# Kernel optimization log

Hardware: AMD Instinct MI355X
Metric: run time of the kernel (lower is better)

Reference implementation:

```python
import jax, jax.numpy as jnp
import numpy as np

D_MODEL = 1024
D_FF = 286
NUM_REL = 2
EPS = 1e-6


def setup_inputs() -> dict:
    key = jax.random.key(0)
    ks = jax.random.split(key, 8)
    N, E = 20000, 320000
    hidden_states = jax.random.normal(ks[0], (N, D_MODEL), dtype=jnp.float32)
    edge_index = jax.random.randint(ks[1], (2, E), 0, N, dtype=jnp.int64)
    edge_type = jax.random.randint(ks[2], (E,), 0, NUM_REL, dtype=jnp.int64)
    # learned parameters
    ln_weight = jnp.ones((D_MODEL,), dtype=jnp.float32)
    W_rel = jax.random.normal(ks[3], (NUM_REL, D_MODEL, D_FF), dtype=jnp.float32) * (1.0 / np.sqrt(D_MODEL))
    W_root = jax.random.normal(ks[4], (D_MODEL, D_FF), dtype=jnp.float32) * (1.0 / np.sqrt(D_MODEL))
    conv_bias = jnp.zeros((D_FF,), dtype=jnp.float32)
    wo_weight = jax.random.normal(ks[5], (D_FF, D_MODEL), dtype=jnp.float32) * (1.0 / np.sqrt(D_FF))
    return {"hidden_states": hidden_states, "edge_index": edge_index, "edge_type": edge_type,
            "ln_weight": ln_weight, "W_rel": W_rel, "W_root": W_root,
            "conv_bias": conv_bias, "wo_weight": wo_weight}


def t5_layer_norm(x, weight):
    # T5-style: RMS only, no mean subtraction, no bias; variance in fp32
    var = jnp.mean(jnp.square(x.astype(jnp.float32)), axis=-1, keepdims=True)
    return weight * (x * jax.lax.rsqrt(var + EPS))


def rgcn_conv(x, edge_index, edge_type, W_rel, W_root, bias):
    # PyG RGCNConv with aggr='mean' per relation, root weight, bias.
    N = x.shape[0]
    src, dst = edge_index[0], edge_index[1]
    h_src = x[src]  # [E, d_model] gather
    out = x @ W_root + bias  # root term, [N, d_ff]
    for r in range(NUM_REL):
        w = (edge_type == r).astype(x.dtype)  # [E]
        msg = (h_src @ W_rel[r]) * w[:, None]  # [E, d_ff]
        sums = jax.ops.segment_sum(msg, dst, num_segments=N)  # [N, d_ff]
        cnt = jax.ops.segment_sum(w, dst, num_segments=N)  # [N]
        out = out + sums / jnp.maximum(cnt, 1.0)[:, None]
    return out


def reference(hidden_states, edge_index, edge_type, ln_weight, W_rel, W_root, conv_bias, wo_weight):
    norm_x = t5_layer_norm(hidden_states, ln_weight)
    y = jax.nn.elu(rgcn_conv(norm_x, edge_index, edge_type, W_rel, W_root, conv_bias))
    # dropout layers are identity in eval mode
    y = y @ wo_weight  # [N, d_model], Linear(d_ff, d_model, bias=False)
    return hidden_states + y
```

## Files before the change

kernel.cpp:

```cpp
#include <hip/hip_runtime.h>
#include <hip/hip_bf16.h>


typedef __bf16  bf16x8  __attribute__((ext_vector_type(8)));
typedef float   floatx4 __attribute__((ext_vector_type(4)));

#define NNODE   20000
#define DMODEL  1024
#define DFF     286
#define DFFP    288
#define NDW     144
#define NPAIR   72

typedef __attribute__((address_space(1))) const void* gptr_t;
typedef __attribute__((address_space(3))) void*       lptr_t;

struct alignas(8) bf4 { __bf16 x, y, z, w; };

__device__ __forceinline__ float bflo(unsigned u) {
    union { unsigned u; float f; } c; c.u = u << 16; return c.f;
}
__device__ __forceinline__ float bfhi(unsigned u) {
    union { unsigned u; float f; } c; c.u = u & 0xffff0000u; return c.f;
}
__device__ __forceinline__ unsigned packbf(float a, float b) {
    union { __bf16 h[2]; unsigned u; } c;
    c.h[0] = (__bf16)a; c.h[1] = (__bf16)b; return c.u;
}
__device__ __forceinline__ float elu1(float v) {
    return v > 0.0f ? v : (expf(v) - 1.0f);
}

__global__ __launch_bounds__(256) void k_transpose_cast(
    const float* __restrict__ src, __bf16* __restrict__ dst,
    int K, int N, int Kout, int Nout)
{
    __shared__ float t[32][33];
    int tx = threadIdx.x & 31, ty = threadIdx.x >> 5;
    int k0 = blockIdx.x * 32, n0 = blockIdx.y * 32;
    #pragma unroll
    for (int r = 0; r < 4; ++r) {
        int k = k0 + ty + r * 8, n = n0 + tx;
        t[ty + r * 8][tx] = (k < K && n < N) ? src[(size_t)k * N + n] : 0.0f;
    }
    __syncthreads();
    #pragma unroll
    for (int r = 0; r < 4; ++r) {
        int n = n0 + ty + r * 8, k = k0 + tx;
        if (n < Nout && k < Kout) dst[(size_t)n * Kout + k] = (__bf16)t[tx][ty + r * 8];
    }
}

__global__ __launch_bounds__(256) void k_rmsnorm(
    const float* __restrict__ x, const float* __restrict__ w,
    __bf16* __restrict__ out)
{
    int row = blockIdx.x;
    int t = threadIdx.x;
    float4 v = reinterpret_cast<const float4*>(x + (size_t)row * DMODEL)[t];
    float ss = v.x * v.x + v.y * v.y + v.z * v.z + v.w * v.w;
    #pragma unroll
    for (int off = 32; off; off >>= 1) ss += __shfl_down(ss, off, 64);
    __shared__ float red[4];
    int lane = t & 63, wv = t >> 6;
    if (lane == 0) red[wv] = ss;
    __syncthreads();
    float tot = red[0] + red[1] + red[2] + red[3];
    float scale = rsqrtf(tot * (1.0f / (float)DMODEL) + 1e-6f);
    float4 wv4 = reinterpret_cast<const float4*>(w)[t];
    bf4 o;
    o.x = (__bf16)(v.x * scale * wv4.x);
    o.y = (__bf16)(v.y * scale * wv4.y);
    o.z = (__bf16)(v.z * scale * wv4.z);
    o.w = (__bf16)(v.w * scale * wv4.w);
    reinterpret_cast<bf4*>(out + (size_t)row * DMODEL)[t] = o;
}

__global__ __launch_bounds__(256, 2) void k_gemm1(
    const __bf16* __restrict__ A, const __bf16* __restrict__ Broot,
    const __bf16* __restrict__ Brel, __bf16* __restrict__ P)
{
    const int bid = blockIdx.x;
    const int mt = bid / 3, mz = bid - mt * 3;
    const __bf16* B = (mz == 0) ? Broot : (Brel + (size_t)(mz - 1) * DFFP * DMODEL);
    __bf16* out = P + (size_t)mz * NNODE * DFFP;

    const int m0 = mt * 128;
    const int tid = threadIdx.x;
    const int lane = tid & 63, wave = tid >> 6;
    const int wm = wave >> 1, wn = wave & 1;
    const int quad = lane >> 4, l16 = lane & 15;

    __shared__ __align__(16) __bf16 As[128 * 32];
    __shared__ __align__(16) __bf16 Bs[288 * 32];

    floatx4 zero = {0.f, 0.f, 0.f, 0.f};
    floatx4 acc[4][9];
    #pragma unroll
    for (int i = 0; i < 4; ++i)
        #pragma unroll
        for (int j = 0; j < 9; ++j) acc[i][j] = zero;

    const int crow = lane >> 2;
    const int ccol = (lane & 3) * 8;

    for (int k0 = 0; k0 < DMODEL; k0 += 32) {
        #pragma unroll
        for (int ii = 0; ii < 7; ++ii) {
            int c = wave + ii * 4;
            if (c < 8) {
                int row = c * 16 + crow;
                int grow = m0 + row; if (grow > NNODE - 1) grow = NNODE - 1;
                __builtin_amdgcn_global_load_lds(
                    (gptr_t)(A + (size_t)grow * DMODEL + k0 + ccol),
                    (lptr_t)(As + c * 512), 16, 0, 0);
            } else if (c < 26) {
                int nrow = (c - 8) * 16 + crow;
                __builtin_amdgcn_global_load_lds(
                    (gptr_t)(B + (size_t)nrow * DMODEL + k0 + ccol),
                    (lptr_t)(Bs + (c - 8) * 512), 16, 0, 0);
            }
        }
        __syncthreads();
        bf16x8 af[4], bq[9];
        #pragma unroll
        for (int i = 0; i < 4; ++i)
            af[i] = *reinterpret_cast<const bf16x8*>(As + (wm * 64 + i * 16 + l16) * 32 + quad * 8);
        #pragma unroll
        for (int j = 0; j < 9; ++j)
            bq[j] = *reinterpret_cast<const bf16x8*>(Bs + (wn * 144 + j * 16 + l16) * 32 + quad * 8);
        #pragma unroll
        for (int i = 0; i < 4; ++i)
            #pragma unroll
            for (int j = 0; j < 9; ++j)
                acc[i][j] = __builtin_amdgcn_mfma_f32_16x16x32_bf16(af[i], bq[j], acc[i][j], 0, 0, 0);
        __syncthreads();
    }
    #pragma unroll
    for (int i = 0; i < 4; ++i) {
        int rbase = m0 + wm * 64 + i * 16 + quad * 4;
        #pragma unroll
        for (int j = 0; j < 9; ++j) {
            int col = wn * 144 + j * 16 + l16;
            #pragma unroll
            for (int rr = 0; rr < 4; ++rr) {
                int row = rbase + rr;
                if (row < NNODE) out[(size_t)row * DFFP + col] = (__bf16)acc[i][j][rr];
            }
        }
    }
}

__global__ __launch_bounds__(256) void k_hist(
    const int* __restrict__ ei, int* __restrict__ bcnt, int E)
{
    int t = blockIdx.x * 256 + threadIdx.x;
    if (t < E) atomicAdd(&bcnt[ei[E + t]], 1);
}

__global__ __launch_bounds__(1024) void k_scan(
    const int* __restrict__ bcnt, int* __restrict__ boff, int* __restrict__ bcur)
{
    const int CH = 20;
    __shared__ int s[1024];
    int t = threadIdx.x;
    int base = t * CH;
    int loc[CH];
    int sum = 0;
    #pragma unroll
    for (int i = 0; i < CH; ++i) {
        int idx = base + i;
        int v = (idx < NNODE) ? bcnt[idx] : 0;
        loc[i] = sum; sum += v;
    }
    s[t] = sum;
    __syncthreads();
    for (int off = 1; off < 1024; off <<= 1) {
        int v = (t >= off) ? s[t - off] : 0;
        __syncthreads();
        s[t] += v;
        __syncthreads();
    }
    int prev = (t == 0) ? 0 : s[t - 1];
    #pragma unroll
    for (int i = 0; i < CH; ++i) {
        int idx = base + i;
        if (idx < NNODE) { int o = prev + loc[i]; boff[idx] = o; bcur[idx] = o; }
    }
    if (t == 1023) boff[NNODE] = s[1023];
}

__global__ __launch_bounds__(256) void k_scatter_idx(
    const int* __restrict__ ei, const int* __restrict__ et,
    int* __restrict__ bcur, int* __restrict__ sorted, int E)
{
    int t = blockIdx.x * 256 + threadIdx.x;
    if (t >= E) return;
    int src = ei[t], dst = ei[E + t], r = et[t];
    int pos = atomicAdd(&bcur[dst], 1);
    sorted[pos] = src | (r << 20);
}

__global__ __launch_bounds__(256) void k_reduce(
    const int* __restrict__ boff, const int* __restrict__ sorted,
    const __bf16* __restrict__ proj, const float* __restrict__ bias,
    __bf16* __restrict__ y2)
{
    int b = blockIdx.x * 4 + (threadIdx.x >> 6);
    int lane = threadIdx.x & 63;
    int start = boff[b], end = boff[b + 1];
    bool t8 = lane < 8;

    const uint2* base1 = reinterpret_cast<const uint2*>(proj + (size_t)NNODE * DFFP);
    const uint2* base2 = reinterpret_cast<const uint2*>(proj + (size_t)2 * NNODE * DFFP);

    float a0[4] = {0.f, 0.f, 0.f, 0.f}, a0t[4] = {0.f, 0.f, 0.f, 0.f};
    float a1[4] = {0.f, 0.f, 0.f, 0.f}, a1t[4] = {0.f, 0.f, 0.f, 0.f};
    int c0 = 0, c1 = 0;
    uint2 zz; zz.x = 0u; zz.y = 0u;

    int e = start;
    for (; e + 2 <= end; e += 2) {
        int p0 = sorted[e], p1 = sorted[e + 1];
        int r0i = p0 >> 20, r1i = p1 >> 20;
        const uint2* r0 = (r0i ? base2 : base1) + (size_t)(p0 & 0xFFFFF) * NPAIR;
        const uint2* r1 = (r1i ? base2 : base1) + (size_t)(p1 & 0xFFFFF) * NPAIR;
        uint2 x0 = r0[lane];
        uint2 x1 = r1[lane];
        uint2 y0 = t8 ? r0[64 + lane] : zz;
        uint2 y1 = t8 ? r1[64 + lane] : zz;
        if (r0i) {
            a1[0] += bflo(x0.x); a1[1] += bfhi(x0.x); a1[2] += bflo(x0.y); a1[3] += bfhi(x0.y);
            a1t[0] += bflo(y0.x); a1t[1] += bfhi(y0.x); a1t[2] += bflo(y0.y); a1t[3] += bfhi(y0.y);
            ++c1;
        } else {
            a0[0] += bflo(x0.x); a0[1] += bfhi(x0.x); a0[2] += bflo(x0.y); a0[3] += bfhi(x0.y);
            a0t[0] += bflo(y0.x); a0t[1] += bfhi(y0.x); a0t[2] += bflo(y0.y); a0t[3] += bfhi(y0.y);
            ++c0;
        }
        if (r1i) {
            a1[0] += bflo(x1.x); a1[1] += bfhi(x1.x); a1[2] += bflo(x1.y); a1[3] += bfhi(x1.y);
            a1t[0] += bflo(y1.x); a1t[1] += bfhi(y1.x); a1t[2] += bflo(y1.y); a1t[3] += bfhi(y1.y);
            ++c1;
        } else {
            a0[0] += bflo(x1.x); a0[1] += bfhi(x1.x); a0[2] += bflo(x1.y); a0[3] += bfhi(x1.y);
            a0t[0] += bflo(y1.x); a0t[1] += bfhi(y1.x); a0t[2] += bflo(y1.y); a0t[3] += bfhi(y1.y);
            ++c0;
        }
    }
    if (e < end) {
        int p0 = sorted[e];
        int r0i = p0 >> 20;
        const uint2* r0 = (r0i ? base2 : base1) + (size_t)(p0 & 0xFFFFF) * NPAIR;
        uint2 x0 = r0[lane];
        uint2 y0 = t8 ? r0[64 + lane] : zz;
        if (r0i) {
            a1[0] += bflo(x0.x); a1[1] += bfhi(x0.x); a1[2] += bflo(x0.y); a1[3] += bfhi(x0.y);
            a1t[0] += bflo(y0.x); a1t[1] += bfhi(y0.x); a1t[2] += bflo(y0.y); a1t[3] += bfhi(y0.y);
            ++c1;
        } else {
            a0[0] += bflo(x0.x); a0[1] += bfhi(x0.x); a0[2] += bflo(x0.y); a0[3] += bfhi(x0.y);
            a0t[0] += bflo(y0.x); a0t[1] += bfhi(y0.x); a0t[2] += bflo(y0.y); a0t[3] += bfhi(y0.y);
            ++c0;
        }
    }

    float inv0 = 1.0f / fmaxf((float)c0, 1.0f);
    float inv1 = 1.0f / fmaxf((float)c1, 1.0f);

    const uint2* rootrow = reinterpret_cast<const uint2*>(proj) + (size_t)b * NPAIR;
    uint2* outrow = reinterpret_cast<uint2*>(y2) + (size_t)b * NPAIR;

    {
        uint2 rt = rootrow[lane];
        int f = 4 * lane;
        float v0 = bflo(rt.x) + bias[f]     + a0[0] * inv0 + a1[0] * inv1;
        float v1 = bfhi(rt.x) + bias[f + 1] + a0[1] * inv0 + a1[1] * inv1;
        float v2 = bflo(rt.y) + bias[f + 2] + a0[2] * inv0 + a1[2] * inv1;
        float v3 = bfhi(rt.y) + bias[f + 3] + a0[3] * inv0 + a1[3] * inv1;
        uint2 o; o.x = packbf(elu1(v0), elu1(v1)); o.y = packbf(elu1(v2), elu1(v3));
        outrow[lane] = o;
    }
    if (t8) {
        uint2 rt = rootrow[64 + lane];
        int f = 256 + 4 * lane;
        float b0 = (f     < DFF) ? bias[f]     : 0.0f;
        float b1 = (f + 1 < DFF) ? bias[f + 1] : 0.0f;
        float b2 = (f + 2 < DFF) ? bias[f + 2] : 0.0f;
        float b3 = (f + 3 < DFF) ? bias[f + 3] : 0.0f;
        float v0 = bflo(rt.x) + b0 + a0t[0] * inv0 + a1t[0] * inv1;
        float v1 = bfhi(rt.x) + b1 + a0t[1] * inv0 + a1t[1] * inv1;
        float v2 = bflo(rt.y) + b2 + a0t[2] * inv0 + a1t[2] * inv1;
        float v3 = bfhi(rt.y) + b3 + a0t[3] * inv0 + a1t[3] * inv1;
        uint2 o; o.x = packbf(elu1(v0), elu1(v1)); o.y = packbf(elu1(v2), elu1(v3));
        outrow[64 + lane] = o;
    }
}

__global__ __launch_bounds__(256) void k_gemm2(
    const __bf16* __restrict__ A, const __bf16* __restrict__ Bt,
    const float* __restrict__ hidden, float* __restrict__ out)
{
    const int m0 = blockIdx.x * 128;
    const int n0 = blockIdx.y * 128;
    const int tid = threadIdx.x;
    const int lane = tid & 63, wave = tid >> 6;
    const int wm = wave >> 1, wn = wave & 1;
    const int quad = lane >> 4, l16 = lane & 15;

    __shared__ __align__(16) __bf16 As[128 * 40];
    __shared__ __align__(16) __bf16 Bs[128 * 40];

    floatx4 zero = {0.f, 0.f, 0.f, 0.f};
    floatx4 acc[4][4];
    #pragma unroll
    for (int i = 0; i < 4; ++i)
        #pragma unroll
        for (int j = 0; j < 4; ++j) acc[i][j] = zero;

    for (int k0 = 0; k0 < DFFP; k0 += 32) {
        #pragma unroll
        for (int i = 0; i < 2; ++i) {
            int chunk = tid + i * 256;
            int row = chunk >> 2, col = (chunk & 3) * 8;
            int grow = m0 + row; if (grow > NNODE - 1) grow = NNODE - 1;
            *reinterpret_cast<uint4*>(&As[row * 40 + col]) =
                *reinterpret_cast<const uint4*>(A + (size_t)grow * DFFP + k0 + col);
            *reinterpret_cast<uint4*>(&Bs[row * 40 + col]) =
                *reinterpret_cast<const uint4*>(Bt + (size_t)(n0 + row) * DFFP + k0 + col);
        }
        __syncthreads();
        bf16x8 af[4], bq[4];
        #pragma unroll
        for (int i = 0; i < 4; ++i)
            af[i] = *reinterpret_cast<const bf16x8*>(&As[(wm * 64 + i * 16 + l16) * 40 + quad * 8]);
        #pragma unroll
        for (int j = 0; j < 4; ++j)
            bq[j] = *reinterpret_cast<const bf16x8*>(&Bs[(wn * 64 + j * 16 + l16) * 40 + quad * 8]);
        #pragma unroll
        for (int i = 0; i < 4; ++i)
            #pragma unroll
            for (int j = 0; j < 4; ++j)
                acc[i][j] = __builtin_amdgcn_mfma_f32_16x16x32_bf16(af[i], bq[j], acc[i][j], 0, 0, 0);
        __syncthreads();
    }
    #pragma unroll
    for (int i = 0; i < 4; ++i) {
        int rbase = m0 + wm * 64 + i * 16 + quad * 4;
        #pragma unroll
        for (int j = 0; j < 4; ++j) {
            int col = n0 + wn * 64 + j * 16 + l16;
            #pragma unroll
            for (int rr = 0; rr < 4; ++rr) {
                int row = rbase + rr;
                if (row < NNODE) {
                    size_t idx = (size_t)row * DMODEL + col;
                    out[idx] = hidden[idx] + acc[i][j][rr];
                }
            }
        }
    }
}

extern "C" void kernel_launch(void* const* d_in, const int* in_sizes, int n_in,
                              void* d_out, int out_size, void* d_ws, size_t ws_size,
                              hipStream_t stream)
{
    const float* hidden   = (const float*)d_in[0];
    const int*   ei       = (const int*)  d_in[1];
    const int*   et       = (const int*)  d_in[2];
    const float* ln_w     = (const float*)d_in[3];
    const float* W_rel    = (const float*)d_in[4];
    const float* W_root   = (const float*)d_in[5];
    const float* bias     = (const float*)d_in[6];
    const float* wo       = (const float*)d_in[7];
    float* out = (float*)d_out;

    const int E = in_sizes[1] / 2;

    char* ws = (char*)d_ws;
    __bf16* norm_bf = (__bf16*)(ws + 0);
    __bf16* proj    = (__bf16*)(ws + 40960000);
    __bf16* y2      = (__bf16*)(ws + 75520000);
    __bf16* wroot_t = (__bf16*)(ws + 87040000);
    __bf16* wrel_t  = (__bf16*)(ws + 87629824);
    __bf16* wo_t    = (__bf16*)(ws + 88809472);
    int*    bcnt    = (int*)   (ws + 89399296);
    int*    boff    = (int*)   (ws + 89479296);
    int*    bcur    = (int*)   (ws + 89559312);
    int*    sorted  = (int*)   (ws + 89639312);

    hipMemsetAsync(bcnt, 0, 80000, stream);

    {
        dim3 g1((DMODEL + 31) / 32, (DFFP + 31) / 32);
        k_transpose_cast<<<g1, 256, 0, stream>>>(W_root, wroot_t, DMODEL, DFF, DMODEL, DFFP);
        k_transpose_cast<<<g1, 256, 0, stream>>>(W_rel, wrel_t, DMODEL, DFF, DMODEL, DFFP);
        k_transpose_cast<<<g1, 256, 0, stream>>>(W_rel + (size_t)DMODEL * DFF,
                                                 wrel_t + (size_t)DFFP * DMODEL,
                                                 DMODEL, DFF, DMODEL, DFFP);
        dim3 g2((DFFP + 31) / 32, (DMODEL + 31) / 32);
        k_transpose_cast<<<g2, 256, 0, stream>>>(wo, wo_t, DFF, DMODEL, DFFP, DMODEL);
    }

    k_rmsnorm<<<NNODE, 256, 0, stream>>>(hidden, ln_w, norm_bf);

    k_hist<<<(E + 255) / 256, 256, 0, stream>>>(ei, bcnt, E);
    k_scan<<<1, 1024, 0, stream>>>(bcnt, boff, bcur);
    k_scatter_idx<<<(E + 255) / 256, 256, 0, stream>>>(ei, et, bcur, sorted, E);

    {
        int nmt = (NNODE + 127) / 128;
        k_gemm1<<<nmt * 3, 256, 0, stream>>>(norm_bf, wroot_t, wrel_t, proj);
    }

    k_reduce<<<NNODE / 4, 256, 0, stream>>>(boff, sorted, proj, bias, y2);

    {
        dim3 grid((NNODE + 127) / 128, DMODEL / 128);
        k_gemm2<<<grid, 256, 0, stream>>>(y2, wo_t, hidden, out);
    }
}
```

Before: 383.8 us.

## Double-buffer gemm2 with direct global-to-LDS loads and branchless reduce gather

The output GEMM now stages A and B tiles through double-buffered LDS using global_load_lds, so the next K slice loads while MFMAs run. Half of the residual hidden values are prefetched before the main loop, which hides their latency, and occupancy is hinted at 3 blocks per CU. The edge-reduce kernel replaces per-relation branches with weighted FMAs and unrolls by four to issue more independent gathers. In exchange the LDS layout loses its padding, which may cause bank conflicts, and register pressure goes up.

```diff
diff --git a/kernel.cpp b/kernel.cpp
--- a/kernel.cpp
+++ b/kernel.cpp
@@ -212,61 +212,63 @@
     bool t8 = lane < 8;
 
     const uint2* base1 = reinterpret_cast<const uint2*>(proj + (size_t)NNODE * DFFP);
-    const uint2* base2 = reinterpret_cast<const uint2*>(proj + (size_t)2 * NNODE * DFFP);
-
-    float a0[4] = {0.f, 0.f, 0.f, 0.f}, a0t[4] = {0.f, 0.f, 0.f, 0.f};
-    float a1[4] = {0.f, 0.f, 0.f, 0.f}, a1t[4] = {0.f, 0.f, 0.f, 0.f};
-    int c0 = 0, c1 = 0;
+    const size_t relstride = (size_t)NNODE * NPAIR;
+
+    float a0[4] = {0.f, 0.f, 0.f, 0.f}, b0a[4] = {0.f, 0.f, 0.f, 0.f};
+    float a1[4] = {0.f, 0.f, 0.f, 0.f}, b1a[4] = {0.f, 0.f, 0.f, 0.f};
+    float c0 = 0.f, c1 = 0.f;
     uint2 zz; zz.x = 0u; zz.y = 0u;
 
     int e = start;
-    for (; e + 2 <= end; e += 2) {
-        int p0 = sorted[e], p1 = sorted[e + 1];
-        int r0i = p0 >> 20, r1i = p1 >> 20;
-        const uint2* r0 = (r0i ? base2 : base1) + (size_t)(p0 & 0xFFFFF) * NPAIR;
-        const uint2* r1 = (r1i ? base2 : base1) + (size_t)(p1 & 0xFFFFF) * NPAIR;
-        uint2 x0 = r0[lane];
-        uint2 x1 = r1[lane];
-        uint2 y0 = t8 ? r0[64 + lane] : zz;
-        uint2 y1 = t8 ? r1[64 + lane] : zz;
-        if (r0i) {
-            a1[0] += bflo(x0.x); a1[1] += bfhi(x0.x); a1[2] += bflo(x0.y); a1[3] += bfhi(x0.y);
-            a1t[0] += bflo(y0.x); a1t[1] += bfhi(y0.x); a1t[2] += bflo(y0.y); a1t[3] += bfhi(y0.y);
-            ++c1;
-        } else {
-            a0[0] += bflo(x0.x); a0[1] += bfhi(x0.x); a0[2] += bflo(x0.y); a0[3] += bfhi(x0.y);
-            a0t[0] += bflo(y0.x); a0t[1] += bfhi(y0.x); a0t[2] += bflo(y0.y); a0t[3] += bfhi(y0.y);
-            ++c0;
-        }
-        if (r1i) {
-            a1[0] += bflo(x1.x); a1[1] += bfhi(x1.x); a1[2] += bflo(x1.y); a1[3] += bfhi(x1.y);
-            a1t[0] += bflo(y1.x); a1t[1] += bfhi(y1.x); a1t[2] += bflo(y1.y); a1t[3] += bfhi(y1.y);
-            ++c1;
-        } else {
-            a0[0] += bflo(x1.x); a0[1] += bfhi(x1.x); a0[2] += bflo(x1.y); a0[3] += bfhi(x1.y);
-            a0t[0] += bflo(y1.x); a0t[1] += bfhi(y1.x); a0t[2] += bflo(y1.y); a0t[3] += bfhi(y1.y);
-            ++c0;
-        }
-    }
-    if (e < end) {
-        int p0 = sorted[e];
-        int r0i = p0 >> 20;
-        const uint2* r0 = (r0i ? base2 : base1) + (size_t)(p0 & 0xFFFFF) * NPAIR;
-        uint2 x0 = r0[lane];
-        uint2 y0 = t8 ? r0[64 + lane] : zz;
-        if (r0i) {
-            a1[0] += bflo(x0.x); a1[1] += bfhi(x0.x); a1[2] += bflo(x0.y); a1[3] += bfhi(x0.y);
-            a1t[0] += bflo(y0.x); a1t[1] += bfhi(y0.x); a1t[2] += bflo(y0.y); a1t[3] += bfhi(y0.y);
-            ++c1;
-        } else {
-            a0[0] += bflo(x0.x); a0[1] += bfhi(x0.x); a0[2] += bflo(x0.y); a0[3] += bfhi(x0.y);
-            a0t[0] += bflo(y0.x); a0t[1] += bfhi(y0.x); a0t[2] += bflo(y0.y); a0t[3] += bfhi(y0.y);
-            ++c0;
-        }
-    }
-
-    float inv0 = 1.0f / fmaxf((float)c0, 1.0f);
-    float inv1 = 1.0f / fmaxf((float)c1, 1.0f);
+    for (; e + 4 <= end; e += 4) {
+        uint2 x[4], y[4]; float w1[4];
+        #pragma unroll
+        for (int u = 0; u < 4; ++u) {
+            int p = sorted[e + u];
+            int ri = p >> 20;
+            w1[u] = (float)ri;
+            const uint2* row = base1 + (size_t)(p & 0xFFFFF) * NPAIR + (ri ? relstride : 0);
+            x[u] = row[lane];
+            y[u] = t8 ? row[64 + lane] : zz;
+        }
+        #pragma unroll
+        for (int u = 0; u < 4; ++u) {
+            float W1 = w1[u], W0 = 1.0f - W1;
+            c0 += W0; c1 += W1;
+            float v0 = bflo(x[u].x), v1 = bfhi(x[u].x), v2 = bflo(x[u].y), v3 = bfhi(x[u].y);
+            a0[0] += W0 * v0; a1[0] += W1 * v0;
+            a0[1] += W0 * v1; a1[1] += W1 * v1;
+            a0[2] += W0 * v2; a1[2] += W1 * v2;
+            a0[3] += W0 * v3; a1[3] += W1 * v3;
+            float u0 = bflo(y[u].x), u1 = bfhi(y[u].x), u2 = bflo(y[u].y), u3 = bfhi(y[u].y);
+            b0a[0] += W0 * u0; b1a[0] += W1 * u0;
+            b0a[1] += W0 * u1; b1a[1] += W1 * u1;
+            b0a[2] += W0 * u2; b1a[2] += W1 * u2;
+            b0a[3] += W0 * u3; b1a[3] += W1 * u3;
+        }
+    }
+    for (; e < end; ++e) {
+        int p = sorted[e];
+        int ri = p >> 20;
+        float W1 = (float)ri, W0 = 1.0f - W1;
+        const uint2* row = base1 + (size_t)(p & 0xFFFFF) * NPAIR + (ri ? relstride : 0);
+        uint2 x = row[lane];
+        uint2 y = t8 ? row[64 + lane] : zz;
+        c0 += W0; c1 += W1;
+        float v0 = bflo(x.x), v1 = bfhi(x.x), v2 = bflo(x.y), v3 = bfhi(x.y);
+        a0[0] += W0 * v0; a1[0] += W1 * v0;
+        a0[1] += W0 * v1; a1[1] += W1 * v1;
+        a0[2] += W0 * v2; a1[2] += W1 * v2;
+        a0[3] += W0 * v3; a1[3] += W1 * v3;
+        float u0 = bflo(y.x), u1 = bfhi(y.x), u2 = bflo(y.y), u3 = bfhi(y.y);
+        b0a[0] += W0 * u0; b1a[0] += W1 * u0;
+        b0a[1] += W0 * u1; b1a[1] += W1 * u1;
+        b0a[2] += W0 * u2; b1a[2] += W1 * u2;
+        b0a[3] += W0 * u3; b1a[3] += W1 * u3;
+    }
+
+    float inv0 = 1.0f / fmaxf(c0, 1.0f);
+    float inv1 = 1.0f / fmaxf(c1, 1.0f);
 
     const uint2* rootrow = reinterpret_cast<const uint2*>(proj) + (size_t)b * NPAIR;
     uint2* outrow = reinterpret_cast<uint2*>(y2) + (size_t)b * NPAIR;
@@ -284,20 +286,20 @@
     if (t8) {
         uint2 rt = rootrow[64 + lane];
         int f = 256 + 4 * lane;
-        float b0 = (f     < DFF) ? bias[f]     : 0.0f;
-        float b1 = (f + 1 < DFF) ? bias[f + 1] : 0.0f;
-        float b2 = (f + 2 < DFF) ? bias[f + 2] : 0.0f;
-        float b3 = (f + 3 < DFF) ? bias[f + 3] : 0.0f;
-        float v0 = bflo(rt.x) + b0 + a0t[0] * inv0 + a1t[0] * inv1;
-        float v1 = bfhi(rt.x) + b1 + a0t[1] * inv0 + a1t[1] * inv1;
-        float v2 = bflo(rt.y) + b2 + a0t[2] * inv0 + a1t[2] * inv1;
-        float v3 = bfhi(rt.y) + b3 + a0t[3] * inv0 + a1t[3] * inv1;
+        float g0 = (f     < DFF) ? bias[f]     : 0.0f;
+        float g1 = (f + 1 < DFF) ? bias[f + 1] : 0.0f;
+        float g2 = (f + 2 < DFF) ? bias[f + 2] : 0.0f;
+        float g3 = (f + 3 < DFF) ? bias[f + 3] : 0.0f;
+        float v0 = bflo(rt.x) + g0 + b0a[0] * inv0 + b1a[0] * inv1;
+        float v1 = bfhi(rt.x) + g1 + b0a[1] * inv0 + b1a[1] * inv1;
+        float v2 = bflo(rt.y) + g2 + b0a[2] * inv0 + b1a[2] * inv1;
+        float v3 = bfhi(rt.y) + g3 + b0a[3] * inv0 + b1a[3] * inv1;
         uint2 o; o.x = packbf(elu1(v0), elu1(v1)); o.y = packbf(elu1(v2), elu1(v3));
         outrow[64 + lane] = o;
     }
 }
 
-__global__ __launch_bounds__(256) void k_gemm2(
+__global__ __launch_bounds__(256, 3) void k_gemm2(
     const __bf16* __restrict__ A, const __bf16* __restrict__ Bt,
     const float* __restrict__ hidden, float* __restrict__ out)
 {
@@ -308,8 +310,21 @@
     const int wm = wave >> 1, wn = wave & 1;
     const int quad = lane >> 4, l16 = lane & 15;
 
-    __shared__ __align__(16) __bf16 As[128 * 40];
-    __shared__ __align__(16) __bf16 Bs[128 * 40];
+    __shared__ __align__(16) __bf16 As[2][128 * 32];
+    __shared__ __align__(16) __bf16 Bs[2][128 * 32];
+
+    float hv[2][4][4];
+    #pragma unroll
+    for (int i = 0; i < 2; ++i) {
+        #pragma unroll
+        for (int rr = 0; rr < 4; ++rr) {
+            int row = m0 + wm * 64 + i * 16 + quad * 4 + rr;
+            if (row > NNODE - 1) row = NNODE - 1;
+            const float* hrow = hidden + (size_t)row * DMODEL + n0 + wn * 64 + l16;
+            #pragma unroll
+            for (int j = 0; j < 4; ++j) hv[i][j][rr] = hrow[j * 16];
+        }
+    }
 
     floatx4 zero = {0.f, 0.f, 0.f, 0.f};
     floatx4 acc[4][4];
@@ -318,25 +333,38 @@
         #pragma unroll
         for (int j = 0; j < 4; ++j) acc[i][j] = zero;
 
-    for (int k0 = 0; k0 < DFFP; k0 += 32) {
-        #pragma unroll
-        for (int i = 0; i < 2; ++i) {
-            int chunk = tid + i * 256;
-            int row = chunk >> 2, col = (chunk & 3) * 8;
-            int grow = m0 + row; if (grow > NNODE - 1) grow = NNODE - 1;
-            *reinterpret_cast<uint4*>(&As[row * 40 + col]) =
-                *reinterpret_cast<const uint4*>(A + (size_t)grow * DFFP + k0 + col);
-            *reinterpret_cast<uint4*>(&Bs[row * 40 + col]) =
-                *reinterpret_cast<const uint4*>(Bt + (size_t)(n0 + row) * DFFP + k0 + col);
-        }
-        __syncthreads();
+    const int crow = lane >> 2, ccol = (lane & 3) * 8;
+
+    auto stage = [&](int kk, int buf) {
+        #pragma unroll
+        for (int ii = 0; ii < 4; ++ii) {
+            int c = wave + ii * 4;
+            if (c < 8) {
+                int grow = m0 + c * 16 + crow; if (grow > NNODE - 1) grow = NNODE - 1;
+                __builtin_amdgcn_global_load_lds(
+                    (gptr_t)(A + (size_t)grow * DFFP + kk + ccol),
+                    (lptr_t)(As[buf] + c * 512), 16, 0, 0);
+            } else {
+                int nrow = n0 + (c - 8) * 16 + crow;
+                __builtin_amdgcn_global_load_lds(
+                    (gptr_t)(Bt + (size_t)nrow * DFFP + kk + ccol),
+                    (lptr_t)(Bs[buf] + (c - 8) * 512), 16, 0, 0);
+            }
+        }
+    };
+
+    stage(0, 0);
+    __syncthreads();
+    for (int ks = 0; ks < 9; ++ks) {
+        int buf = ks & 1;
+        if (ks < 8) stage((ks + 1) * 32, buf ^ 1);
         bf16x8 af[4], bq[4];
         #pragma unroll
         for (int i = 0; i < 4; ++i)
-            af[i] = *reinterpret_cast<const bf16x8*>(&As[(wm * 64 + i * 16 + l16) * 40 + quad * 8]);
+            af[i] = *reinterpret_cast<const bf16x8*>(As[buf] + (wm * 64 + i * 16 + l16) * 32 + quad * 8);
         #pragma unroll
         for (int j = 0; j < 4; ++j)
-            bq[j] = *reinterpret_cast<const bf16x8*>(&Bs[(wn * 64 + j * 16 + l16) * 40 + quad * 8]);
+            bq[j] = *reinterpret_cast<const bf16x8*>(Bs[buf] + (wn * 64 + j * 16 + l16) * 32 + quad * 8);
         #pragma unroll
         for (int i = 0; i < 4; ++i)
             #pragma unroll
@@ -344,8 +372,22 @@
                 acc[i][j] = __builtin_amdgcn_mfma_f32_16x16x32_bf16(af[i], bq[j], acc[i][j], 0, 0, 0);
         __syncthreads();
     }
-    #pragma unroll
-    for (int i = 0; i < 4; ++i) {
+
+    float hw[2][4][4];
+    #pragma unroll
+    for (int i = 0; i < 2; ++i) {
+        #pragma unroll
+        for (int rr = 0; rr < 4; ++rr) {
+            int row = m0 + wm * 64 + (i + 2) * 16 + quad * 4 + rr;
+            if (row > NNODE - 1) row = NNODE - 1;
+            const float* hrow = hidden + (size_t)row * DMODEL + n0 + wn * 64 + l16;
+            #pragma unroll
+            for (int j = 0; j < 4; ++j) hw[i][j][rr] = hrow[j * 16];
+        }
+    }
+
+    #pragma unroll
+    for (int i = 0; i < 2; ++i) {
         int rbase = m0 + wm * 64 + i * 16 + quad * 4;
         #pragma unroll
         for (int j = 0; j < 4; ++j) {
@@ -353,10 +395,22 @@
             #pragma unroll
             for (int rr = 0; rr < 4; ++rr) {
                 int row = rbase + rr;
-                if (row < NNODE) {
-                    size_t idx = (size_t)row * DMODEL + col;
-                    out[idx] = hidden[idx] + acc[i][j][rr];
-                }
+                if (row < NNODE)
+                    out[(size_t)row * DMODEL + col] = hv[i][j][rr] + acc[i][j][rr];
+            }
+        }
+    }
+    #pragma unroll
+    for (int i = 2; i < 4; ++i) {
+        int rbase = m0 + wm * 64 + i * 16 + quad * 4;
+        #pragma unroll
+        for (int j = 0; j < 4; ++j) {
+            int col = n0 + wn * 64 + j * 16 + l16;
+            #pragma unroll
+            for (int rr = 0; rr < 4; ++rr) {
+                int row = rbase + rr;
+                if (row < NNODE)
+                    out[(size_t)row * DMODEL + col] = hw[i - 2][j][rr] + acc[i][j][rr];
             }
         }
     }
```

Measured after the change: 382.7 us. Within noise of the previous version (-0.3%).
